# Kernel tuning notes

Hardware: AMD Instinct MI355X
Metric: run time of the kernel (lower is better)

## Reference

```python
import jax, jax.numpy as jnp
import numpy as np

# ---- config (matches init_kwargs) ----
CLIP_FRAMES, CLIP_STRIDE = 1, 2
CODEBOOK_SIZE, CODEBOOK_DIM = 1024, 512
WORD_SIZE = CODEBOOK_SIZE // 4
VOCAB = 3000
LAMBDA_MMD, LAMBDA_SIM = 0.1, 1.0


def conv3d(x, w, b, pad):
    # x: (N,C,T,H,W), w: (O,I,kt,kh,kw)
    out = jax.lax.conv_general_dilated(x, w, (1, 1, 1), [(p, p) for p in pad],
                                       dimension_numbers=('NCDHW', 'OIDHW', 'NCDHW'))
    return out + b[None, :, None, None, None]


def bn_relu(x, g, b, nc):
    # training-mode BatchNorm3d, stats computed per clip-batch (over B,T,H,W),
    # matching the torch loop that calls the encoder once per clip.
    s = x.shape
    xr = x.reshape((nc, s[0] // nc) + s[1:])
    m = xr.mean(axis=(1, 3, 4, 5), keepdims=True)
    v = xr.var(axis=(1, 3, 4, 5), keepdims=True)
    xn = (xr - m) * jax.lax.rsqrt(v + 1e-5)
    xn = xn * g[None, None, :, None, None, None] + b[None, None, :, None, None, None]
    return jax.nn.relu(xn).reshape(s)


def maxpool_hw(x):
    return jax.lax.reduce_window(x, -jnp.inf, jax.lax.max,
                                 (1, 1, 1, 2, 2), (1, 1, 1, 2, 2), 'VALID')


def gru_layer(x, w_ih, w_hh, b_ih, b_hh):
    # PyTorch GRU cell math; x: (B,L,D) -> (B,L,H)
    B = x.shape[0]
    H = w_hh.shape[1]

    def step(h, xt):
        gi = xt @ w_ih.T + b_ih
        gh = h @ w_hh.T + b_hh
        i_r, i_z, i_n = jnp.split(gi, 3, axis=-1)
        h_r, h_z, h_n = jnp.split(gh, 3, axis=-1)
        r = jax.nn.sigmoid(i_r + h_r)
        z = jax.nn.sigmoid(i_z + h_z)
        n = jnp.tanh(i_n + r * h_n)
        hn = (1.0 - z) * n + z * h
        return hn, hn

    h0 = jnp.zeros((B, H), x.dtype)
    _, ys = jax.lax.scan(step, h0, jnp.swapaxes(x, 0, 1))
    return jnp.swapaxes(ys, 0, 1)


def nearest_code(flat, book):
    # squared euclidean distance; argmin identical to torch.cdist(p=2)+argmin
    d2 = (flat * flat).sum(-1, keepdims=True) - 2.0 * flat @ book.T + (book * book).sum(-1)
    return jnp.argmin(d2, axis=-1)


def _forward(videos, conv1_w, conv1_b, bn1_g, bn1_b, conv2_w, conv2_b, bn2_g, bn2_b,
             conv3_w, conv3_b, bn3_g, bn3_b, tconv_w, tconv_b, bn4_g, bn4_b,
             proj_w, proj_b, codebook, word_codebook, align_w, align_b,
             gru_wih0, gru_whh0, gru_bih0, gru_bhh0, gru_wih1, gru_whh1, gru_bih1, gru_bhh1,
             dec1_w, dec1_b, dec2_w, dec2_b, dec3_w, dec3_b, text_tokens):
    sg = jax.lax.stop_gradient
    B, _, T, Hh, Ww = videos.shape
    nc = (T - CLIP_FRAMES) // CLIP_STRIDE + 1
    # gather all clips, fold clip dim into batch for the convs
    idx = jnp.arange(nc)[:, None] * CLIP_STRIDE + jnp.arange(CLIP_FRAMES)[None]
    clips = jnp.transpose(videos[:, :, idx], (2, 0, 1, 3, 4, 5))  # (nc,B,3,cf,H,W)
    x = clips.reshape(nc * B, 3, CLIP_FRAMES, Hh, Ww)
    x = maxpool_hw(bn_relu(conv3d(x, conv1_w, conv1_b, (1, 1, 1)), bn1_g, bn1_b, nc))
    x = maxpool_hw(bn_relu(conv3d(x, conv2_w, conv2_b, (1, 1, 1)), bn2_g, bn2_b, nc))
    x = bn_relu(conv3d(x, conv3_w, conv3_b, (1, 1, 1)), bn3_g, bn3_b, nc)
    # AdaptiveAvgPool3d((CLIP_FRAMES,4,4)): T already CLIP_FRAMES, H,W divisible by 4
    N, C, Tc, Hc, Wc = x.shape
    x = x.reshape(N, C, Tc, 4, Hc // 4, 4, Wc // 4).mean(axis=(4, 6))
    x = bn_relu(conv3d(x, tconv_w, tconv_b, (1, 0, 0)), bn4_g, bn4_b, nc)
    feats = jnp.transpose(x.reshape(nc, B, -1), (1, 0, 2))  # (B, nc, 256*cf*16)
    features = feats @ proj_w.T + proj_b                     # (B, nc, D)
    D = features.shape[-1]
    # --- VQ quantize ---
    flat = features.reshape(-1, D)
    tok = nearest_code(flat, codebook)
    quantized = codebook[tok].reshape(B, nc, D)
    commitment = jnp.mean((features - sg(quantized)) ** 2)
    codebook_loss = jnp.mean((quantized - sg(features)) ** 2)
    h = gru_layer(quantized[:, :-1], gru_wih0, gru_whh0, gru_bih0, gru_bhh0)
    h = gru_layer(h, gru_wih1, gru_whh1, gru_bih1, gru_bhh1)
    context_loss = jnp.mean((h - features[:, 1:]) ** 2)
    vq_loss = commitment + 0.25 * codebook_loss + 0.1 * context_loss
    # --- SimpleCRA: mean of char pairs -> nearest word code ---
    wsrc = quantized.reshape(B, nc // 2, 2, D).mean(axis=2)
    widx = nearest_code(wsrc.reshape(-1, D), word_codebook).reshape(B, nc // 2)
    wemb = word_codebook[widx]  # (B, nw, D)
    flat_w = wemb.reshape(-1, D)
    alignment = jnp.mean((flat_w @ align_w.T + align_b - sg(flat_w)) ** 2)
    # --- translation: mean word context -> MLP decoder -> CE vs first token, summed over batch ---
    ctx = wemb.mean(axis=1)  # (B, D)
    hh = jax.nn.relu(ctx @ dec1_w.T + dec1_b)
    hh = jax.nn.relu(hh @ dec2_w.T + dec2_b)  # dropout = identity (eval)
    logits = hh @ dec3_w.T + dec3_b           # (B, VOCAB)
    logp = jax.nn.log_softmax(logits, axis=-1)
    translation = -jnp.take_along_axis(logp, text_tokens[:, :1], axis=1).sum()
    total = vq_loss + LAMBDA_MMD * alignment + LAMBDA_SIM * translation
    return widx, total


def setup_inputs() -> dict:
    key = jax.random.key(0)
    ks = iter(jax.random.split(key, 48))

    def rn(shape, scale):
        return jax.random.normal(next(ks), shape, jnp.float32) * scale

    D = CODEBOOK_DIM
    inp = {}
    inp['videos'] = jax.random.normal(next(ks), (4, 3, 32, 64, 64), jnp.float32)
    inp['conv1_w'] = rn((64, 3, 3, 3, 3), 0.15); inp['conv1_b'] = jnp.zeros((64,), jnp.float32)
    inp['bn1_g'] = jnp.ones((64,), jnp.float32); inp['bn1_b'] = jnp.zeros((64,), jnp.float32)
    inp['conv2_w'] = rn((128, 64, 3, 3, 3), 0.034); inp['conv2_b'] = jnp.zeros((128,), jnp.float32)
    inp['bn2_g'] = jnp.ones((128,), jnp.float32); inp['bn2_b'] = jnp.zeros((128,), jnp.float32)
    inp['conv3_w'] = rn((256, 128, 3, 3, 3), 0.024); inp['conv3_b'] = jnp.zeros((256,), jnp.float32)
    inp['bn3_g'] = jnp.ones((256,), jnp.float32); inp['bn3_b'] = jnp.zeros((256,), jnp.float32)
    inp['tconv_w'] = rn((256, 256, 3, 1, 1), 0.05); inp['tconv_b'] = jnp.zeros((256,), jnp.float32)
    inp['bn4_g'] = jnp.ones((256,), jnp.float32); inp['bn4_b'] = jnp.zeros((256,), jnp.float32)
    inp['proj_w'] = rn((D, 256 * CLIP_FRAMES * 16), 0.02); inp['proj_b'] = jnp.zeros((D,), jnp.float32)
    inp['codebook'] = jax.random.uniform(next(ks), (CODEBOOK_SIZE, D), jnp.float32,
                                         -1.0 / CODEBOOK_SIZE, 1.0 / CODEBOOK_SIZE)
    inp['word_codebook'] = jax.random.uniform(next(ks), (WORD_SIZE, D), jnp.float32,
                                              -1.0 / WORD_SIZE, 1.0 / WORD_SIZE)
    inp['align_w'] = rn((D, D), 0.04); inp['align_b'] = jnp.zeros((D,), jnp.float32)
    for l in (0, 1):
        inp[f'gru_wih{l}'] = rn((3 * D, D), 0.044)
        inp[f'gru_whh{l}'] = rn((3 * D, D), 0.044)
        inp[f'gru_bih{l}'] = jnp.zeros((3 * D,), jnp.float32)
        inp[f'gru_bhh{l}'] = jnp.zeros((3 * D,), jnp.float32)
    inp['dec1_w'] = rn((512, D), 0.044); inp['dec1_b'] = jnp.zeros((512,), jnp.float32)
    inp['dec2_w'] = rn((1024, 512), 0.044); inp['dec2_b'] = jnp.zeros((1024,), jnp.float32)
    inp['dec3_w'] = rn((VOCAB, 1024), 0.031); inp['dec3_b'] = jnp.zeros((VOCAB,), jnp.float32)
    inp['text_tokens'] = jax.random.randint(next(ks), (4, 10), 0, VOCAB)
    return inp


def reference(videos, conv1_w, conv1_b, bn1_g, bn1_b, conv2_w, conv2_b, bn2_g, bn2_b,
              conv3_w, conv3_b, bn3_g, bn3_b, tconv_w, tconv_b, bn4_g, bn4_b,
              proj_w, proj_b, codebook, word_codebook, align_w, align_b,
              gru_wih0, gru_whh0, gru_bih0, gru_bhh0, gru_wih1, gru_whh1, gru_bih1, gru_bhh1,
              dec1_w, dec1_b, dec2_w, dec2_b, dec3_w, dec3_b, text_tokens):
    return _forward(videos, conv1_w, conv1_b, bn1_g, bn1_b, conv2_w, conv2_b, bn2_g, bn2_b,
                    conv3_w, conv3_b, bn3_g, bn3_b, tconv_w, tconv_b, bn4_g, bn4_b,
                    proj_w, proj_b, codebook, word_codebook, align_w, align_b,
                    gru_wih0, gru_whh0, gru_bih0, gru_bhh0, gru_wih1, gru_whh1, gru_bih1, gru_bhh1,
                    dec1_w, dec1_b, dec2_w, dec2_b, dec3_w, dec3_b, text_tokens)
```

## Files before the change

kernel.cpp:

```cpp
#include <hip/hip_runtime.h>


static const size_t OFF_X1P  = 0;
static const size_t OFF_Y2   = 4194304;
static const size_t OFF_X2P  = 0;
static const size_t OFF_Y3   = 4194304;
static const size_t OFF_Y3P1 = 8388608;
static const size_t OFF_X3P  = 2097152;
static const size_t OFF_Y4   = 2359296;
static const size_t OFF_X4   = 2621440;
static const size_t OFF_FEAT = 2883584;
static const size_t OFF_QUANT= 2916352;
static const size_t OFF_GI1  = 2949120;
static const size_t OFF_GI2  = 3047424;
static const size_t OFF_H1   = 3145728;
static const size_t OFF_H2   = 3178496;
static const size_t OFF_WEMB = 3211264;
static const size_t OFF_CTX  = 3227648;
static const size_t OFF_HH1  = 3229696;
static const size_t OFF_HH2  = 3231744;
static const size_t OFF_LOG  = 3235840;
static const size_t OFF_PP   = 3247840;
static const size_t OFF_SC    = 12582912;
static const size_t OFF_SH    = 12587008;
static const size_t OFF_ACCP  = 12591104;
static const size_t OFF_COMMIT= 12623872;
static const size_t OFF_CTXA  = 12623936;
static const size_t OFF_ALIGNA= 12624056;

__global__ __launch_bounds__(256) void k_conv1_stats3(
        const float* __restrict__ videos, const float* __restrict__ w1,
        const float* __restrict__ b1, float* __restrict__ accP) {
    __shared__ float sP[3 * 18 * 66];
    __shared__ float wsm[3 * 9 * 16];
    __shared__ float sRed[4][16], qRed[4][16];
    int oc0 = blockIdx.x * 16, rq = blockIdx.y, n = blockIdx.z;
    int c = n >> 2, b = n & 3;
    int tid = threadIdx.x;
    int rp = tid >> 5, cq = tid & 31;
    for (int e = tid; e < 3564; e += 256) {
        int ic = e / 1188, rem = e % 1188;
        int r = rem / 66, col = rem % 66;
        int gr = rq * 16 - 1 + r, gc = col - 1;
        float v = 0.f;
        if (gr >= 0 && gr < 64 && gc >= 0 && gc < 64)
            v = videos[((size_t)(b * 3 + ic) * 32 + 2 * c) * 4096 + gr * 64 + gc];
        sP[e] = v;
    }
    for (int e = tid; e < 432; e += 256) {
        int ic = e / 144, rem = e % 144, k = rem / 16, j = rem % 16;
        wsm[e] = w1[((size_t)((oc0 + j) * 3 + ic) * 3 + 1) * 9 + k];
    }
    __syncthreads();
    float acc[4][16];
#pragma unroll
    for (int p = 0; p < 4; ++p)
#pragma unroll
        for (int j = 0; j < 16; ++j) acc[p][j] = 0.f;
#pragma unroll
    for (int ic = 0; ic < 3; ++ic) {
        const float* base = &sP[ic * 1188 + (2 * rp) * 66 + 2 * cq];
        float patch[4][4];
#pragma unroll
        for (int r = 0; r < 4; ++r)
#pragma unroll
            for (int q = 0; q < 4; ++q) patch[r][q] = base[r * 66 + q];
#pragma unroll
        for (int k = 0; k < 9; ++k) {
            int kr = k / 3, kc = k % 3;
            float4 w0 = *(const float4*)&wsm[(ic * 9 + k) * 16 + 0];
            float4 w1v = *(const float4*)&wsm[(ic * 9 + k) * 16 + 4];
            float4 w2 = *(const float4*)&wsm[(ic * 9 + k) * 16 + 8];
            float4 w3 = *(const float4*)&wsm[(ic * 9 + k) * 16 + 12];
#pragma unroll
            for (int p = 0; p < 4; ++p) {
                float vv = patch[(p >> 1) + kr][(p & 1) + kc];
                acc[p][0]  += vv * w0.x; acc[p][1]  += vv * w0.y;
                acc[p][2]  += vv * w0.z; acc[p][3]  += vv * w0.w;
                acc[p][4]  += vv * w1v.x; acc[p][5]  += vv * w1v.y;
                acc[p][6]  += vv * w1v.z; acc[p][7]  += vv * w1v.w;
                acc[p][8]  += vv * w2.x; acc[p][9]  += vv * w2.y;
                acc[p][10] += vv * w2.z; acc[p][11] += vv * w2.w;
                acc[p][12] += vv * w3.x; acc[p][13] += vv * w3.y;
                acc[p][14] += vv * w3.z; acc[p][15] += vv * w3.w;
            }
        }
    }
    int lane = tid & 63, wave = tid >> 6;
#pragma unroll
    for (int j = 0; j < 16; ++j) {
        float bj = b1[oc0 + j];
        float s = 0.f, q = 0.f;
#pragma unroll
        for (int p = 0; p < 4; ++p) {
            float a = acc[p][j] + bj;
            s += a; q += a * a;
        }
#pragma unroll
        for (int m = 1; m < 64; m <<= 1) {
            s += __shfl_xor(s, m);
            q += __shfl_xor(q, m);
        }
        if (lane == 0) { sRed[wave][j] = s; qRed[wave][j] = q; }
    }
    __syncthreads();
    if (tid < 16) {
        float s = ((sRed[0][tid] + sRed[1][tid]) + (sRed[2][tid] + sRed[3][tid]));
        float q = ((qRed[0][tid] + qRed[1][tid]) + (qRed[2][tid] + qRed[3][tid]));
        int oc = oc0 + tid;
        size_t slot = (((size_t)(c * 64 + oc)) * 4 + b) * 4 + rq;
        accP[slot] = s;
        accP[16384 + slot] = q;
    }
}

__global__ void k_conv1_fin(const float* __restrict__ accP, const float* __restrict__ g1,
                            const float* __restrict__ be1, float* __restrict__ sc,
                            float* __restrict__ sh) {
    int e = blockIdx.x * 256 + threadIdx.x;
    if (e >= 1024) return;
    int oc = e & 63;
    const float* ps = accP + (size_t)e * 16;
    const float* pq = accP + 16384 + (size_t)e * 16;
    float s = 0.f, q = 0.f;
#pragma unroll
    for (int i = 0; i < 16; ++i) { s += ps[i]; q += pq[i]; }
    float m = s * (1.f / 16384.f);
    float var = q * (1.f / 16384.f) - m * m;
    float sf = g1[oc] * rsqrtf(var + 1e-5f);
    sc[e] = sf;
    sh[e] = be1[oc] - m * sf;
}

__global__ __launch_bounds__(256) void k_conv1_apply3(
        const float* __restrict__ videos, const float* __restrict__ w1,
        const float* __restrict__ b1, const float* __restrict__ sc,
        const float* __restrict__ sh, float* __restrict__ x1p) {
    __shared__ float sP[3 * 18 * 66];
    __shared__ float wsm[3 * 9 * 16];
    int oc0 = blockIdx.x * 16, rq = blockIdx.y, n = blockIdx.z;
    int c = n >> 2, b = n & 3;
    int tid = threadIdx.x;
    int rp = tid >> 5, cq = tid & 31;
    for (int e = tid; e < 3564; e += 256) {
        int ic = e / 1188, rem = e % 1188;
        int r = rem / 66, col = rem % 66;
        int gr = rq * 16 - 1 + r, gc = col - 1;
        float v = 0.f;
        if (gr >= 0 && gr < 64 && gc >= 0 && gc < 64)
            v = videos[((size_t)(b * 3 + ic) * 32 + 2 * c) * 4096 + gr * 64 + gc];
        sP[e] = v;
    }
    for (int e = tid; e < 432; e += 256) {
        int ic = e / 144, rem = e % 144, k = rem / 16, j = rem % 16;
        wsm[e] = w1[((size_t)((oc0 + j) * 3 + ic) * 3 + 1) * 9 + k];
    }
    __syncthreads();
    float acc[4][16];
#pragma unroll
    for (int p = 0; p < 4; ++p)
#pragma unroll
        for (int j = 0; j < 16; ++j) acc[p][j] = 0.f;
#pragma unroll
    for (int ic = 0; ic < 3; ++ic) {
        const float* base = &sP[ic * 1188 + (2 * rp) * 66 + 2 * cq];
        float patch[4][4];
#pragma unroll
        for (int r = 0; r < 4; ++r)
#pragma unroll
            for (int q = 0; q < 4; ++q) patch[r][q] = base[r * 66 + q];
#pragma unroll
        for (int k = 0; k < 9; ++k) {
            int kr = k / 3, kc = k % 3;
            float4 w0 = *(const float4*)&wsm[(ic * 9 + k) * 16 + 0];
            float4 w1v = *(const float4*)&wsm[(ic * 9 + k) * 16 + 4];
            float4 w2 = *(const float4*)&wsm[(ic * 9 + k) * 16 + 8];
            float4 w3 = *(const float4*)&wsm[(ic * 9 + k) * 16 + 12];
#pragma unroll
            for (int p = 0; p < 4; ++p) {
                float vv = patch[(p >> 1) + kr][(p & 1) + kc];
                acc[p][0]  += vv * w0.x; acc[p][1]  += vv * w0.y;
                acc[p][2]  += vv * w0.z; acc[p][3]  += vv * w0.w;
                acc[p][4]  += vv * w1v.x; acc[p][5]  += vv * w1v.y;
                acc[p][6]  += vv * w1v.z; acc[p][7]  += vv * w1v.w;
                acc[p][8]  += vv * w2.x; acc[p][9]  += vv * w2.y;
                acc[p][10] += vv * w2.z; acc[p][11] += vv * w2.w;
                acc[p][12] += vv * w3.x; acc[p][13] += vv * w3.y;
                acc[p][14] += vv * w3.z; acc[p][15] += vv * w3.w;
            }
        }
    }
#pragma unroll
    for (int j = 0; j < 16; ++j) {
        int oc = oc0 + j;
        float bj = b1[oc];
        float scj = sc[c * 64 + oc], shj = sh[c * 64 + oc];
        float m = -1e30f;
#pragma unroll
        for (int p = 0; p < 4; ++p) m = fmaxf(m, (acc[p][j] + bj) * scj + shj);
        x1p[((size_t)n * 64 + oc) * 1024 + (rq * 8 + rp) * 32 + cq] = fmaxf(m, 0.f);
    }
}

__global__ __launch_bounds__(256) void k_conv2(
        const float* __restrict__ in, const float* __restrict__ wt,
        const float* __restrict__ bias, float* __restrict__ out) {
    __shared__ __align__(16) float sIn[8 * 10 * 36];
    __shared__ __align__(16) float sW[8 * 9 * 32];
    int oc0 = blockIdx.x * 32, r0 = blockIdx.y * 8, n = blockIdx.z;
    int tid = threadIdx.x;
    int ocq = tid >> 5;
    int rg = (tid >> 3) & 3;
    int cg = tid & 7;
    float acc[4][8];
#pragma unroll
    for (int j = 0; j < 4; ++j)
#pragma unroll
        for (int p = 0; p < 8; ++p) acc[j][p] = 0.f;

    for (int ic0 = 0; ic0 < 64; ic0 += 8) {
        __syncthreads();
        for (int e = tid; e < 2720; e += 256) {
            int ch = e / 340, rem = e % 340;
            int r = rem / 34, col = rem % 34;
            int gr = r0 - 1 + r, gc = col - 1;
            float v = 0.f;
            if (gr >= 0 && gr < 32 && gc >= 0 && gc < 32)
                v = in[((size_t)(n * 64 + ic0 + ch) * 32 + gr) * 32 + gc];
            sIn[ch * 360 + r * 36 + col] = v;
        }
        for (int e = tid; e < 2304; e += 256) {
            int c = e / 288, r1 = e % 288, k = r1 / 32, j = r1 % 32;
            sW[e] = wt[((size_t)(oc0 + j) * 64 + ic0 + c) * 27 + 9 + k];
        }
        __syncthreads();
        for (int c = 0; c < 8; ++c) {
            const float* base = &sIn[c * 360 + (2 * rg) * 36 + 4 * cg];
            float patch[4][6];
#pragma unroll
            for (int r = 0; r < 4; ++r) {
                float4 p4 = *(const float4*)&base[r * 36];
                float2 p2 = *(const float2*)&base[r * 36 + 4];
                patch[r][0] = p4.x; patch[r][1] = p4.y; patch[r][2] = p4.z;
                patch[r][3] = p4.w; patch[r][4] = p2.x; patch[r][5] = p2.y;
            }
#pragma unroll
            for (int k = 0; k < 9; ++k) {
                int kr = k / 3, kc = k % 3;
                float4 w4 = *(const float4*)&sW[c * 288 + k * 32 + ocq * 4];
#pragma unroll
                for (int p = 0; p < 8; ++p) {
                    int pr = p >> 2, pcq = p & 3;
                    float vv = patch[pr + kr][pcq + kc];
                    acc[0][p] += vv * w4.x; acc[1][p] += vv * w4.y;
                    acc[2][p] += vv * w4.z; acc[3][p] += vv * w4.w;
                }
            }
        }
    }
#pragma unroll
    for (int j = 0; j < 4; ++j) {
        int oc = oc0 + ocq * 4 + j;
        float bj = bias[oc];
#pragma unroll
        for (int pr = 0; pr < 2; ++pr) {
            float4 o4 = make_float4(acc[j][pr * 4 + 0] + bj, acc[j][pr * 4 + 1] + bj,
                                    acc[j][pr * 4 + 2] + bj, acc[j][pr * 4 + 3] + bj);
            *(float4*)&out[((size_t)(n * 128 + oc) * 32 + r0 + 2 * rg + pr) * 32 + 4 * cg] = o4;
        }
    }
}

__global__ __launch_bounds__(256) void k_conv3p(
        const float* __restrict__ in, const float* __restrict__ wt,
        float* __restrict__ outP) {
    __shared__ __align__(16) float sIn[8 * 18 * 20];
    __shared__ __align__(16) float sW[8 * 9 * 32];
    int oc0 = blockIdx.x * 32, n = blockIdx.y, half = blockIdx.z;
    int tid = threadIdx.x;
    int ocq = tid >> 5;
    int rg = (tid >> 2) & 7;
    int cg = tid & 3;
    float acc[4][8];
#pragma unroll
    for (int j = 0; j < 4; ++j)
#pragma unroll
        for (int p = 0; p < 8; ++p) acc[j][p] = 0.f;

    int icB = half * 64;
    for (int ic0 = icB; ic0 < icB + 64; ic0 += 8) {
        __syncthreads();
        for (int e = tid; e < 2592; e += 256) {
            int ch = e / 324, rem = e % 324;
            int r = rem / 18, cc = rem % 18;
            int gr = r - 1, gc = cc - 1;
            float v = 0.f;
            if (gr >= 0 && gr < 16 && gc >= 0 && gc < 16)
                v = in[((size_t)(n * 128 + ic0 + ch) * 16 + gr) * 16 + gc];
            sIn[ch * 360 + r * 20 + cc] = v;
        }
        for (int e = tid; e < 2304; e += 256) {
            int c = e / 288, r1 = e % 288, k = r1 / 32, j = r1 % 32;
            sW[e] = wt[((size_t)(oc0 + j) * 128 + ic0 + c) * 27 + 9 + k];
        }
        __syncthreads();
        for (int c = 0; c < 8; ++c) {
            const float* base = &sIn[c * 360 + (2 * rg) * 20 + 4 * cg];
            float patch[4][6];
#pragma unroll
            for (int r = 0; r < 4; ++r) {
                float4 p4 = *(const float4*)&base[r * 20];
                float2 p2 = *(const float2*)&base[r * 20 + 4];
                patch[r][0] = p4.x; patch[r][1] = p4.y; patch[r][2] = p4.z;
                patch[r][3] = p4.w; patch[r][4] = p2.x; patch[r][5] = p2.y;
            }
#pragma unroll
            for (int k = 0; k < 9; ++k) {
                int kr = k / 3, kc = k % 3;
                float4 w4 = *(const float4*)&sW[c * 288 + k * 32 + ocq * 4];
#pragma unroll
                for (int p = 0; p < 8; ++p) {
                    int pr = p >> 2, pcq = p & 3;
                    float vv = patch[pr + kr][pcq + kc];
                    acc[0][p] += vv * w4.x; acc[1][p] += vv * w4.y;
                    acc[2][p] += vv * w4.z; acc[3][p] += vv * w4.w;
                }
            }
        }
    }
    float* dst = outP + (size_t)half * 4194304;
#pragma unroll
    for (int j = 0; j < 4; ++j) {
        int oc = oc0 + ocq * 4 + j;
#pragma unroll
        for (int pr = 0; pr < 2; ++pr) {
            float4 o4 = make_float4(acc[j][pr * 4 + 0], acc[j][pr * 4 + 1],
                                    acc[j][pr * 4 + 2], acc[j][pr * 4 + 3]);
            *(float4*)&dst[((size_t)(n * 256 + oc) * 16 + 2 * rg + pr) * 16 + 4 * cg] = o4;
        }
    }
}

__global__ void k_bn_stats3p(const float* __restrict__ P, const float* __restrict__ bias,
                             const float* __restrict__ g, const float* __restrict__ be,
                             float* __restrict__ scale, float* __restrict__ shift) {
    int c = blockIdx.x, ch = blockIdx.y, tid = threadIdx.x;
    float bj = bias[ch];
    float s = 0.f, s2 = 0.f;
    for (int b = 0; b < 4; ++b) {
        size_t base = ((size_t)(c * 4 + b) * 256 + ch) * 256;
        for (int i = tid; i < 256; i += 256) {
            size_t idx = base + i;
            float v = (P[idx] + P[idx + 4194304]) + bj;
            s += v; s2 += v * v;
        }
    }
    __shared__ float rs[256], rq[256];
    rs[tid] = s; rq[tid] = s2; __syncthreads();
    for (int k = 128; k > 0; k >>= 1) {
        if (tid < k) { rs[tid] += rs[tid + k]; rq[tid] += rq[tid + k]; }
        __syncthreads();
    }
    if (tid == 0) {
        float inv = 1.f / 1024.f;
        float m = rs[0] * inv, var = rq[0] * inv - m * m;
        float sc = g[ch] * rsqrtf(var + 1e-5f);
        scale[c * 256 + ch] = sc;
        shift[c * 256 + ch] = be[ch] - m * sc;
    }
}

__global__ void k_bn_apply_avgpool4p(const float* __restrict__ P, const float* __restrict__ bias,
                                     const float* __restrict__ scale, const float* __restrict__ shift,
                                     float* __restrict__ out) {
    size_t idx = (size_t)blockIdx.x * 256 + threadIdx.x;
    int j = (int)(idx & 3), i = (int)(idx >> 2) & 3;
    int ch = (int)(idx >> 4) & 255, n = (int)(idx >> 12);
    int c = n >> 2;
    float bj = bias[ch];
    float sc = scale[c * 256 + ch], sh = shift[c * 256 + ch];
    size_t base = (((size_t)n * 256 + ch) * 16 + i * 4) * 16 + j * 4;
    float s = 0.f;
#pragma unroll
    for (int r = 0; r < 4; ++r)
#pragma unroll
        for (int q = 0; q < 4; ++q) {
            size_t pidx = base + r * 16 + q;
            float v = (P[pidx] + P[pidx + 4194304]) + bj;
            s += fmaxf(v * sc + sh, 0.f);
        }
    out[idx] = s * (1.f / 16.f);
}

__global__ void k_bn_stats(const float* __restrict__ buf, const float* __restrict__ g,
                           const float* __restrict__ be, float* __restrict__ scale,
                           float* __restrict__ shift, int C, int HW) {
    int c = blockIdx.x, ch = blockIdx.y, tid = threadIdx.x;
    float s = 0.f, s2 = 0.f;
    for (int b = 0; b < 4; ++b) {
        const float* p = buf + ((size_t)(c * 4 + b) * C + ch) * HW;
        for (int i = tid; i < HW; i += 256) { float v = p[i]; s += v; s2 += v * v; }
    }
    __shared__ float rs[256], rq[256];
    rs[tid] = s; rq[tid] = s2; __syncthreads();
    for (int k = 128; k > 0; k >>= 1) {
        if (tid < k) { rs[tid] += rs[tid + k]; rq[tid] += rq[tid + k]; }
        __syncthreads();
    }
    if (tid == 0) {
        float inv = 1.f / (float)(4 * HW);
        float m = rs[0] * inv, var = rq[0] * inv - m * m;
        float sc = g[ch] * rsqrtf(var + 1e-5f);
        scale[c * C + ch] = sc;
        shift[c * C + ch] = be[ch] - m * sc;
    }
}

__global__ void k_bn_apply_pool(const float* __restrict__ in, const float* __restrict__ scale,
                                const float* __restrict__ shift, float* __restrict__ out,
                                int C, int H, int W) {
    int OH = H >> 1, OW = W >> 1;
    size_t idx = (size_t)blockIdx.x * 256 + threadIdx.x;
    int ow = (int)(idx % OW);
    size_t r = idx / OW;
    int oh = (int)(r % OH); r /= OH;
    int ch = (int)(r % C);
    int n = (int)(r / C);
    int c = n >> 2;
    float sc = scale[c * C + ch], sh = shift[c * C + ch];
    const float* p = in + (((size_t)n * C + ch) * H + 2 * oh) * W + 2 * ow;
    float m = 0.f;
    m = fmaxf(m, p[0] * sc + sh);
    m = fmaxf(m, p[1] * sc + sh);
    m = fmaxf(m, p[W] * sc + sh);
    m = fmaxf(m, p[W + 1] * sc + sh);
    out[idx] = m;
}

__global__ void k_tconv(const float* __restrict__ x3p, const float* __restrict__ tw,
                        const float* __restrict__ tb, float* __restrict__ y4) {
    size_t idx = (size_t)blockIdx.x * 256 + threadIdx.x;
    int p = (int)(idx & 15), o = (int)(idx >> 4) & 255, n = (int)(idx >> 12);
    const float* xr = x3p + (size_t)n * 4096 + p;
    float a = tb[o];
    for (int i = 0; i < 256; ++i) a += xr[i * 16] * tw[((size_t)o * 256 + i) * 3 + 1];
    y4[idx] = a;
}

__global__ void k_bn_apply(const float* __restrict__ in, const float* __restrict__ scale,
                           const float* __restrict__ shift, float* __restrict__ out) {
    size_t idx = (size_t)blockIdx.x * 256 + threadIdx.x;
    int ch = (int)(idx >> 4) & 255, n = (int)(idx >> 12);
    int c = n >> 2;
    float sc = scale[c * 256 + ch], sh = shift[c * 256 + ch];
    out[idx] = fmaxf(in[idx] * sc + sh, 0.f);
}

__global__ __launch_bounds__(256) void k_proj_part(
        const float* __restrict__ A, const float* __restrict__ B, float* __restrict__ PP) {
    __shared__ __align__(16) float As[64 * 68];
    __shared__ __align__(16) float Bs[64 * 68];
    int n0 = blockIdx.x * 64, ks = blockIdx.y;
    int tid = threadIdx.x, tm = tid >> 4, tn = tid & 15;
    float acc[4][4];
#pragma unroll
    for (int i = 0; i < 4; ++i)
#pragma unroll
        for (int j = 0; j < 4; ++j) acc[i][j] = 0.f;
    int kb = ks * 512;
    for (int k0 = kb; k0 < kb + 512; k0 += 64) {
        __syncthreads();
        for (int e = tid; e < 4096; e += 256) {
            int m = e >> 6, k = e & 63;
            As[k * 68 + m] = A[(size_t)m * 4096 + k0 + k];
            Bs[k * 68 + m] = B[(size_t)(n0 + m) * 4096 + k0 + k];
        }
        __syncthreads();
        for (int k = 0; k < 64; ++k) {
            float4 a4 = *(const float4*)&As[k * 68 + tm * 4];
            float4 b4 = *(const float4*)&Bs[k * 68 + tn * 4];
            acc[0][0] += a4.x * b4.x; acc[0][1] += a4.x * b4.y;
            acc[0][2] += a4.x * b4.z; acc[0][3] += a4.x * b4.w;
            acc[1][0] += a4.y * b4.x; acc[1][1] += a4.y * b4.y;
            acc[1][2] += a4.y * b4.z; acc[1][3] += a4.y * b4.w;
            acc[2][0] += a4.z * b4.x; acc[2][1] += a4.z * b4.y;
            acc[2][2] += a4.z * b4.z; acc[2][3] += a4.z * b4.w;
            acc[3][0] += a4.w * b4.x; acc[3][1] += a4.w * b4.y;
            acc[3][2] += a4.w * b4.z; acc[3][3] += a4.w * b4.w;
        }
    }
#pragma unroll
    for (int i = 0; i < 4; ++i)
#pragma unroll
        for (int j = 0; j < 4; ++j)
            PP[((size_t)(ks * 64 + tm * 4 + i)) * 512 + n0 + tn * 4 + j] = acc[i][j];
}

__global__ void k_proj_fin(const float* __restrict__ PP, const float* __restrict__ pb,
                           float* __restrict__ feat) {
    int e = blockIdx.x * 256 + threadIdx.x;
    int n = e & 511;
    int m = e >> 9;
    float s = pb[n];
#pragma unroll
    for (int ks = 0; ks < 8; ++ks) s += PP[(size_t)ks * 32768 + e];
    int c = m >> 2, b = m & 3;
    int ro = b * 16 + c;
    feat[(size_t)ro * 512 + n] = s;
}

__global__ void k_vq(const float* __restrict__ feat, const float* __restrict__ cb,
                     float* __restrict__ quant, float* __restrict__ commitArr) {
    int row = blockIdx.x, tid = threadIdx.x;
    __shared__ float f[512];
    for (int k = tid; k < 512; k += 256) f[k] = feat[(size_t)row * 512 + k];
    __syncthreads();
    float best = 3.4e38f; int bidx = 0;
    for (int j = tid; j < 1024; j += 256) {
        const float* c = cb + (size_t)j * 512;
        float d2 = 0.f;
        for (int k = 0; k < 512; ++k) { float t = f[k] - c[k]; d2 += t * t; }
        if (d2 < best) { best = d2; bidx = j; }
    }
    __shared__ float rd[256]; __shared__ int ri[256];
    rd[tid] = best; ri[tid] = bidx; __syncthreads();
    for (int k = 128; k > 0; k >>= 1) {
        if (tid < k) {
            float od = rd[tid + k]; int oi = ri[tid + k];
            if (od < rd[tid] || (od == rd[tid] && oi < ri[tid])) { rd[tid] = od; ri[tid] = oi; }
        }
        __syncthreads();
    }
    __shared__ int wsel;
    if (tid == 0) { wsel = ri[0]; commitArr[row] = rd[0]; }
    __syncthreads();
    const float* c = cb + (size_t)wsel * 512;
    for (int k = tid; k < 512; k += 256) quant[(size_t)row * 512 + k] = c[k];
}

__device__ __forceinline__ void gru_gi_one(
        const float* __restrict__ xsRow, const float* __restrict__ wih,
        const float* __restrict__ bih, float* __restrict__ gi, int row, int d) {
    const float4* xp = (const float4*)xsRow;
    const float4* wr = (const float4*)(wih + (size_t)d * 512);
    float a0 = 0.f, a1 = 0.f, a2 = 0.f, a3 = 0.f;
    for (int i = 0; i < 128; i += 4) {
        float4 w0 = wr[i], w1 = wr[i + 1], w2 = wr[i + 2], w3 = wr[i + 3];
        float4 x0 = xp[i], x1 = xp[i + 1], x2 = xp[i + 2], x3 = xp[i + 3];
        a0 += w0.x * x0.x + w0.y * x0.y + w0.z * x0.z + w0.w * x0.w;
        a1 += w1.x * x1.x + w1.y * x1.y + w1.z * x1.z + w1.w * x1.w;
        a2 += w2.x * x2.x + w2.y * x2.y + w2.z * x2.z + w2.w * x2.w;
        a3 += w3.x * x3.x + w3.y * x3.y + w3.z * x3.z + w3.w * x3.w;
    }
    gi[(size_t)row * 1536 + d] = (a0 + a1) + (a2 + a3) + bih[d];
}

__device__ __forceinline__ void gru_step_body(
        const float* __restrict__ gi, const float* __restrict__ whh,
        const float* __restrict__ bhh, float* __restrict__ hseq, int t, int blk) {
    int wv = threadIdx.x >> 6, lane = threadIdx.x & 63;
    int d = blk * 4 + wv;
    const float4* w0p = (const float4*)(whh + (size_t)d * 512);
    const float4* w1p = (const float4*)(whh + (size_t)(512 + d) * 512);
    const float4* w2p = (const float4*)(whh + (size_t)(1024 + d) * 512);
    float4 w0a = w0p[lane * 2], w0b = w0p[lane * 2 + 1];
    float4 w1a = w1p[lane * 2], w1b = w1p[lane * 2 + 1];
    float4 w2a = w2p[lane * 2], w2b = w2p[lane * 2 + 1];
    float bh0 = bhh[d], bh1 = bhh[512 + d], bh2 = bhh[1024 + d];
    for (int b = 0; b < 4; ++b) {
        float4 ha = make_float4(0, 0, 0, 0), hb = ha;
        float hpd = 0.f;
        if (t > 0) {
            const float4* hp = (const float4*)(hseq + (size_t)(b * 16 + t - 1) * 512);
            ha = hp[lane * 2]; hb = hp[lane * 2 + 1];
            hpd = hseq[(size_t)(b * 16 + t - 1) * 512 + d];
        }
        float s0 = w0a.x * ha.x + w0a.y * ha.y + w0a.z * ha.z + w0a.w * ha.w
                 + w0b.x * hb.x + w0b.y * hb.y + w0b.z * hb.z + w0b.w * hb.w;
        float s1 = w1a.x * ha.x + w1a.y * ha.y + w1a.z * ha.z + w1a.w * ha.w
                 + w1b.x * hb.x + w1b.y * hb.y + w1b.z * hb.z + w1b.w * hb.w;
        float s2 = w2a.x * ha.x + w2a.y * ha.y + w2a.z * ha.z + w2a.w * ha.w
                 + w2b.x * hb.x + w2b.y * hb.y + w2b.z * hb.z + w2b.w * hb.w;
#pragma unroll
        for (int m = 1; m < 64; m <<= 1) {
            s0 += __shfl_xor(s0, m);
            s1 += __shfl_xor(s1, m);
            s2 += __shfl_xor(s2, m);
        }
        const float* gr = gi + (size_t)(b * 16 + t) * 1536;
        float rr = 1.f / (1.f + expf(-(gr[d] + s0 + bh0)));
        float zz = 1.f / (1.f + expf(-(gr[512 + d] + s1 + bh1)));
        float nn = tanhf(gr[1024 + d] + rr * (s2 + bh2));
        if (lane == 0)
            hseq[(size_t)(b * 16 + t) * 512 + d] = (1.f - zz) * nn + zz * hpd;
    }
}

__global__ void k_gru_gi6(const float* __restrict__ x, const float* __restrict__ wih,
                          const float* __restrict__ bih, float* __restrict__ gi) {
    int g = blockIdx.x;
    int r = g / 6, part = g % 6;
    int b = r / 15, t = r % 15;
    int row = b * 16 + t;
    __shared__ float xsRow[512];
    for (int k = threadIdx.x; k < 512; k += 256) xsRow[k] = x[(size_t)row * 512 + k];
    __syncthreads();
    gru_gi_one(xsRow, wih, bih, gi, row, part * 256 + threadIdx.x);
}

__global__ __launch_bounds__(256) void k_gru_pipe(
        const float* __restrict__ gi1, const float* __restrict__ whh0,
        const float* __restrict__ bhh0, float* __restrict__ h1,
        const float* __restrict__ wih1, const float* __restrict__ bih1,
        float* __restrict__ gi2, const float* __restrict__ whh1,
        const float* __restrict__ bhh1, float* __restrict__ h2, int t) {
    int bid = blockIdx.x;
    if (bid < 128) {
        if (t < 15) gru_step_body(gi1, whh0, bhh0, h1, t, bid);
    } else if (bid < 256) {
        if (t >= 2) gru_step_body(gi2, whh1, bhh1, h2, t - 2, bid - 128);
    } else {
        if (t >= 1 && t <= 15) {
            int local = bid - 256;
            int b = local / 6, part = local % 6;
            int row = b * 16 + (t - 1);
            __shared__ float xsRow[512];
            for (int k = threadIdx.x; k < 512; k += 256)
                xsRow[k] = h1[(size_t)row * 512 + k];
            __syncthreads();
            gru_gi_one(xsRow, wih1, bih1, gi2, row, part * 256 + threadIdx.x);
        }
    }
}

__global__ void k_ctx_loss(const float* __restrict__ h2, const float* __restrict__ feat,
                           float* __restrict__ ctxArr) {
    int tid = threadIdx.x;
    size_t idx = (size_t)blockIdx.x * 256 + tid;
    int d = (int)(idx & 511);
    int rt = (int)(idx >> 9);
    int t = rt % 15, b = rt / 15;
    float diff = h2[(size_t)(b * 16 + t) * 512 + d] - feat[(size_t)(b * 16 + t + 1) * 512 + d];
    float v = diff * diff;
#pragma unroll
    for (int m = 1; m < 64; m <<= 1) v += __shfl_xor(v, m);
    __shared__ float ws[4];
    if ((tid & 63) == 0) ws[tid >> 6] = v;
    __syncthreads();
    if (tid == 0) ctxArr[blockIdx.x] = ((ws[0] + ws[1]) + (ws[2] + ws[3]));
}

__global__ void k_word_vq(const float* __restrict__ quant, const float* __restrict__ wcb,
                          float* __restrict__ wemb, float* __restrict__ out_widx) {
    int row = blockIdx.x;
    int b = row >> 3, wi = row & 7;
    int tid = threadIdx.x;
    __shared__ float f[512];
    for (int k = tid; k < 512; k += 256)
        f[k] = 0.5f * (quant[(size_t)(b * 16 + 2 * wi) * 512 + k] +
                       quant[(size_t)(b * 16 + 2 * wi + 1) * 512 + k]);
    __syncthreads();
    const float* cp = wcb + (size_t)tid * 512;
    float d2 = 0.f;
    for (int k = 0; k < 512; ++k) { float t = f[k] - cp[k]; d2 += t * t; }
    __shared__ float rd[256]; __shared__ int ri[256];
    rd[tid] = d2; ri[tid] = tid; __syncthreads();
    for (int k = 128; k > 0; k >>= 1) {
        if (tid < k) {
            float od = rd[tid + k]; int oi = ri[tid + k];
            if (od < rd[tid] || (od == rd[tid] && oi < ri[tid])) { rd[tid] = od; ri[tid] = oi; }
        }
        __syncthreads();
    }
    __shared__ int wsel;
    if (tid == 0) { wsel = ri[0]; out_widx[row] = (float)ri[0]; }
    __syncthreads();
    const float* cb = wcb + (size_t)wsel * 512;
    for (int k = tid; k < 512; k += 256) wemb[(size_t)row * 512 + k] = cb[k];
}

__global__ void k_align(const float* __restrict__ wemb, const float* __restrict__ aw,
                        const float* __restrict__ ab, float* __restrict__ alignArr) {
    int row = blockIdx.x, tid = threadIdx.x;
    __shared__ float e[512];
    for (int k = tid; k < 512; k += 256) e[k] = wemb[(size_t)row * 512 + k];
    __syncthreads();
    float local = 0.f;
    for (int d = tid; d < 512; d += 256) {
        const float* wr = aw + (size_t)d * 512;
        float a = ab[d] - e[d];
        for (int k = 0; k < 512; ++k) a += e[k] * wr[k];
        local += a * a;
    }
    __shared__ float rs[256];
    rs[tid] = local; __syncthreads();
    for (int k = 128; k > 0; k >>= 1) { if (tid < k) rs[tid] += rs[tid + k]; __syncthreads(); }
    if (tid == 0) alignArr[row] = rs[0];
}

__global__ void k_ctx(const float* __restrict__ wemb, float* __restrict__ ctx) {
    int e = blockIdx.x * 256 + threadIdx.x;
    int b = e >> 9, d = e & 511;
    float s = 0.f;
#pragma unroll
    for (int wi = 0; wi < 8; ++wi) s += wemb[(size_t)(b * 8 + wi) * 512 + d];
    ctx[e] = s * 0.125f;
}

__global__ void k_smallM(const float* __restrict__ A, const float* __restrict__ B,
                         const float* __restrict__ bias, float* __restrict__ C,
                         int N, int K, int relu) {
    __shared__ float xs[4096];
    int tid = threadIdx.x;
    for (int e = tid; e < 4 * K; e += 256) xs[e] = A[e];
    __syncthreads();
    int r = tid >> 4, kt = tid & 15;
    int n = blockIdx.x * 16 + r;
    float acc[4] = {0, 0, 0, 0};
    if (n < N) {
        int iters = K >> 6;
        for (int i = 0; i < iters; ++i) {
            int k = i * 64 + kt * 4;
            float4 w = *(const float4*)&B[(size_t)n * K + k];
#pragma unroll
            for (int b = 0; b < 4; ++b) {
                float4 x = *(const float4*)&xs[b * K + k];
                acc[b] += w.x * x.x + w.y * x.y + w.z * x.z + w.w * x.w;
            }
        }
    }
#pragma unroll
    for (int b = 0; b < 4; ++b) {
#pragma unroll
        for (int m = 1; m < 16; m <<= 1) acc[b] += __shfl_xor(acc[b], m);
    }
    if (kt == 0 && n < N) {
#pragma unroll
        for (int b = 0; b < 4; ++b) {
            float v = acc[b] + bias[n];
            if (relu) v = fmaxf(v, 0.f);
            C[(size_t)b * N + n] = v;
        }
    }
}

__global__ void k_final(const float* __restrict__ logits, const int* __restrict__ tokens,
                        const float* __restrict__ commitArr, const float* __restrict__ ctxArr,
                        const float* __restrict__ alignArr, float* __restrict__ out_total) {
    int tid = threadIdx.x;
    __shared__ float rs[256];
    __shared__ float sM;
    float tr = 0.f;
    for (int b = 0; b < 4; ++b) {
        const float* lg = logits + (size_t)b * 3000;
        float m = -1e30f;
        for (int d = tid; d < 3000; d += 256) m = fmaxf(m, lg[d]);
        rs[tid] = m; __syncthreads();
        for (int k = 128; k > 0; k >>= 1) { if (tid < k) rs[tid] = fmaxf(rs[tid], rs[tid + k]); __syncthreads(); }
        if (tid == 0) sM = rs[0];
        __syncthreads();
        float M = sM;
        float s = 0.f;
        for (int d = tid; d < 3000; d += 256) s += expf(lg[d] - M);
        rs[tid] = s; __syncthreads();
        for (int k = 128; k > 0; k >>= 1) { if (tid < k) rs[tid] += rs[tid + k]; __syncthreads(); }
        if (tid == 0) {
            int t0 = tokens[b * 10];
            tr += -(lg[t0] - M - logf(rs[0]));
        }
        __syncthreads();
    }
    if (tid == 0) {
        float c0 = 0.f;
        for (int i = 0; i < 64; ++i) c0 += commitArr[i];
        float c1 = 0.f;
        for (int i = 0; i < 120; ++i) c1 += ctxArr[i];
        float c2 = 0.f;
        for (int i = 0; i < 32; ++i) c2 += alignArr[i];
        float total = 1.25f * c0 * (1.f / 32768.f)
                    + 0.1f  * c1 * (1.f / 30720.f)
                    + 0.1f  * c2 * (1.f / 16384.f)
                    + tr;
        *out_total = total;
    }
}

extern "C" void kernel_launch(void* const* d_in, const int* in_sizes, int n_in,
                              void* d_out, int out_size, void* d_ws, size_t ws_size,
                              hipStream_t stream) {
    (void)in_sizes; (void)n_in; (void)out_size; (void)ws_size;
    const float* videos   = (const float*)d_in[0];
    const float* conv1_w  = (const float*)d_in[1];
    const float* conv1_b  = (const float*)d_in[2];
    const float* bn1_g    = (const float*)d_in[3];
    const float* bn1_b    = (const float*)d_in[4];
    const float* conv2_w  = (const float*)d_in[5];
    const float* conv2_b  = (const float*)d_in[6];
    const float* bn2_g    = (const float*)d_in[7];
    const float* bn2_b    = (const float*)d_in[8];
    const float* conv3_w  = (const float*)d_in[9];
    const float* conv3_b  = (const float*)d_in[10];
    const float* bn3_g    = (const float*)d_in[11];
    const float* bn3_b    = (const float*)d_in[12];
    const float* tconv_w  = (const float*)d_in[13];
    const float* tconv_b  = (const float*)d_in[14];
    const float* bn4_g    = (const float*)d_in[15];
    const float* bn4_b    = (const float*)d_in[16];
    const float* proj_w   = (const float*)d_in[17];
    const float* proj_b   = (const float*)d_in[18];
    const float* codebook = (const float*)d_in[19];
    const float* word_cb  = (const float*)d_in[20];
    const float* align_w  = (const float*)d_in[21];
    const float* align_b  = (const float*)d_in[22];
    const float* gru_wih0 = (const float*)d_in[23];
    const float* gru_whh0 = (const float*)d_in[24];
    const float* gru_bih0 = (const float*)d_in[25];
    const float* gru_bhh0 = (const float*)d_in[26];
    const float* gru_wih1 = (const float*)d_in[27];
    const float* gru_whh1 = (const float*)d_in[28];
    const float* gru_bih1 = (const float*)d_in[29];
    const float* gru_bhh1 = (const float*)d_in[30];
    const float* dec1_w   = (const float*)d_in[31];
    const float* dec1_b   = (const float*)d_in[32];
    const float* dec2_w   = (const float*)d_in[33];
    const float* dec2_b   = (const float*)d_in[34];
    const float* dec3_w   = (const float*)d_in[35];
    const float* dec3_b   = (const float*)d_in[36];
    const int*   tokens   = (const int*)d_in[37];

    float* wsf    = (float*)d_ws;
    float* out    = (float*)d_out;
    float* x1p    = wsf + OFF_X1P;
    float* x2p    = wsf + OFF_X2P;
    float* y2     = wsf + OFF_Y2;
    float* y3     = wsf + OFF_Y3;
    float* x3p    = wsf + OFF_X3P;
    float* y4     = wsf + OFF_Y4;
    float* x4     = wsf + OFF_X4;
    float* feat   = wsf + OFF_FEAT;
    float* quant  = wsf + OFF_QUANT;
    float* gi1    = wsf + OFF_GI1;
    float* gi2    = wsf + OFF_GI2;
    float* h1     = wsf + OFF_H1;
    float* h2     = wsf + OFF_H2;
    float* wemb   = wsf + OFF_WEMB;
    float* ctx    = wsf + OFF_CTX;
    float* hh1    = wsf + OFF_HH1;
    float* hh2    = wsf + OFF_HH2;
    float* logit  = wsf + OFF_LOG;
    float* pp     = wsf + OFF_PP;
    float* sc     = wsf + OFF_SC;
    float* sh     = wsf + OFF_SH;
    float* accP   = wsf + OFF_ACCP;
    float* commitA= wsf + OFF_COMMIT;
    float* ctxA   = wsf + OFF_CTXA;
    float* alignA = wsf + OFF_ALIGNA;

    k_conv1_stats3<<<dim3(4, 4, 64), 256, 0, stream>>>(videos, conv1_w, conv1_b, accP);
    k_conv1_fin<<<4, 256, 0, stream>>>(accP, bn1_g, bn1_b, sc, sh);
    k_conv1_apply3<<<dim3(4, 4, 64), 256, 0, stream>>>(videos, conv1_w, conv1_b, sc, sh, x1p);
    k_conv2<<<dim3(4, 4, 64), 256, 0, stream>>>(x1p, conv2_w, conv2_b, y2);
    k_bn_stats<<<dim3(16, 128), 256, 0, stream>>>(y2, bn2_g, bn2_b, sc, sh, 128, 1024);
    k_bn_apply_pool<<<8192, 256, 0, stream>>>(y2, sc, sh, x2p, 128, 32, 32);
    k_conv3p<<<dim3(8, 64, 2), 256, 0, stream>>>(x2p, conv3_w, y3);
    k_bn_stats3p<<<dim3(16, 256), 256, 0, stream>>>(y3, conv3_b, bn3_g, bn3_b, sc, sh);
    k_bn_apply_avgpool4p<<<1024, 256, 0, stream>>>(y3, conv3_b, sc, sh, x3p);
    k_tconv<<<1024, 256, 0, stream>>>(x3p, tconv_w, tconv_b, y4);
    k_bn_stats<<<dim3(16, 256), 256, 0, stream>>>(y4, bn4_g, bn4_b, sc, sh, 256, 16);
    k_bn_apply<<<1024, 256, 0, stream>>>(y4, sc, sh, x4);
    k_proj_part<<<dim3(8, 8), 256, 0, stream>>>(x4, proj_w, pp);
    k_proj_fin<<<128, 256, 0, stream>>>(pp, proj_b, feat);
    k_vq<<<64, 256, 0, stream>>>(feat, codebook, quant, commitA);
    k_gru_gi6<<<360, 256, 0, stream>>>(quant, gru_wih0, gru_bih0, gi1);
    for (int t = 0; t <= 16; ++t)
        k_gru_pipe<<<280, 256, 0, stream>>>(gi1, gru_whh0, gru_bhh0, h1,
                                            gru_wih1, gru_bih1, gi2,
                                            gru_whh1, gru_bhh1, h2, t);
    k_ctx_loss<<<120, 256, 0, stream>>>(h2, feat, ctxA);
    k_word_vq<<<32, 256, 0, stream>>>(quant, word_cb, wemb, out);
    k_align<<<32, 256, 0, stream>>>(wemb, align_w, align_b, alignA);
    k_ctx<<<8, 256, 0, stream>>>(wemb, ctx);
    k_smallM<<<32, 256, 0, stream>>>(ctx, dec1_w, dec1_b, hh1, 512, 512, 1);
    k_smallM<<<64, 256, 0, stream>>>(hh1, dec2_w, dec2_b, hh2, 1024, 512, 1);
    k_smallM<<<188, 256, 0, stream>>>(hh2, dec3_w, dec3_b, logit, 3000, 1024, 0);
    k_final<<<1, 256, 0, stream>>>(logit, tokens, commitA, ctxA, alignA, out + 32);
}
```

Before: 1.095 ms.

## Fold word-VQ and decoder chain into GRU timestep pipeline kernel

Moves word VQ, alignment loss, context averaging and the three decoder matmuls into extra blocks of the per-timestep GRU pipeline kernel, one stage per timestep. The independent decoder chain then overlaps with the latency-bound GRU recurrence, and six separate kernel launches go away. The cost is a larger grid and more shared memory per block in every GRU step launch, which could slow the critical GRU blocks.

```diff
diff --git a/kernel.cpp b/kernel.cpp
--- a/kernel.cpp
+++ b/kernel.cpp
@@ -596,6 +596,44 @@
     }
 }
 
+__device__ __forceinline__ void dev_smallM(float* xs, const float* __restrict__ A,
+                                           const float* __restrict__ B,
+                                           const float* __restrict__ bias,
+                                           float* __restrict__ C,
+                                           int N, int K, int relu, int blk) {
+    int tid = threadIdx.x;
+    for (int e = tid; e < 4 * K; e += 256) xs[e] = A[e];
+    __syncthreads();
+    int r = tid >> 4, kt = tid & 15;
+    int n = blk * 16 + r;
+    float acc[4] = {0, 0, 0, 0};
+    if (n < N) {
+        int iters = K >> 6;
+        for (int i = 0; i < iters; ++i) {
+            int k = i * 64 + kt * 4;
+            float4 w = *(const float4*)&B[(size_t)n * K + k];
+#pragma unroll
+            for (int b = 0; b < 4; ++b) {
+                float4 x = *(const float4*)&xs[b * K + k];
+                acc[b] += w.x * x.x + w.y * x.y + w.z * x.z + w.w * x.w;
+            }
+        }
+    }
+#pragma unroll
+    for (int b = 0; b < 4; ++b) {
+#pragma unroll
+        for (int m = 1; m < 16; m <<= 1) acc[b] += __shfl_xor(acc[b], m);
+    }
+    if (kt == 0 && n < N) {
+#pragma unroll
+        for (int b = 0; b < 4; ++b) {
+            float v = acc[b] + bias[n];
+            if (relu) v = fmaxf(v, 0.f);
+            C[(size_t)b * N + n] = v;
+        }
+    }
+}
+
 __global__ void k_gru_gi6(const float* __restrict__ x, const float* __restrict__ wih,
                           const float* __restrict__ bih, float* __restrict__ gi) {
     int g = blockIdx.x;
@@ -613,22 +651,98 @@
         const float* __restrict__ bhh0, float* __restrict__ h1,
         const float* __restrict__ wih1, const float* __restrict__ bih1,
         float* __restrict__ gi2, const float* __restrict__ whh1,
-        const float* __restrict__ bhh1, float* __restrict__ h2, int t) {
+        const float* __restrict__ bhh1, float* __restrict__ h2,
+        const float* __restrict__ quant, const float* __restrict__ wcb,
+        float* __restrict__ wemb, float* __restrict__ out_widx,
+        const float* __restrict__ aw, const float* __restrict__ ab,
+        float* __restrict__ alignArr, float* __restrict__ ctxB,
+        const float* __restrict__ dec1_w, const float* __restrict__ dec1_b,
+        float* __restrict__ hh1, const float* __restrict__ dec2_w,
+        const float* __restrict__ dec2_b, float* __restrict__ hh2,
+        const float* __restrict__ dec3_w, const float* __restrict__ dec3_b,
+        float* __restrict__ logit, int t) {
+    __shared__ float shbuf[4096];
+    __shared__ float redf[256];
+    __shared__ int   redi[256];
+    __shared__ int   wsel_s;
     int bid = blockIdx.x;
+    int tid = threadIdx.x;
     if (bid < 128) {
         if (t < 15) gru_step_body(gi1, whh0, bhh0, h1, t, bid);
     } else if (bid < 256) {
         if (t >= 2) gru_step_body(gi2, whh1, bhh1, h2, t - 2, bid - 128);
-    } else {
+    } else if (bid < 280) {
         if (t >= 1 && t <= 15) {
             int local = bid - 256;
             int b = local / 6, part = local % 6;
             int row = b * 16 + (t - 1);
-            __shared__ float xsRow[512];
-            for (int k = threadIdx.x; k < 512; k += 256)
-                xsRow[k] = h1[(size_t)row * 512 + k];
+            for (int k = tid; k < 512; k += 256)
+                shbuf[k] = h1[(size_t)row * 512 + k];
             __syncthreads();
-            gru_gi_one(xsRow, wih1, bih1, gi2, row, part * 256 + threadIdx.x);
+            gru_gi_one(shbuf, wih1, bih1, gi2, row, part * 256 + tid);
+        }
+    } else {
+        int tb = bid - 280;
+        if (t == 0) {
+            if (tb < 32) {
+                int b = tb >> 3, wi = tb & 7;
+                for (int k = tid; k < 512; k += 256)
+                    shbuf[k] = 0.5f * (quant[(size_t)(b * 16 + 2 * wi) * 512 + k] +
+                                       quant[(size_t)(b * 16 + 2 * wi + 1) * 512 + k]);
+                __syncthreads();
+                const float* cp = wcb + (size_t)tid * 512;
+                float d2 = 0.f;
+                for (int k = 0; k < 512; ++k) { float tt = shbuf[k] - cp[k]; d2 += tt * tt; }
+                redf[tid] = d2; redi[tid] = tid; __syncthreads();
+                for (int k = 128; k > 0; k >>= 1) {
+                    if (tid < k) {
+                        float od = redf[tid + k]; int oi = redi[tid + k];
+                        if (od < redf[tid] || (od == redf[tid] && oi < redi[tid])) {
+                            redf[tid] = od; redi[tid] = oi;
+                        }
+                    }
+                    __syncthreads();
+                }
+                if (tid == 0) { wsel_s = redi[0]; out_widx[tb] = (float)redi[0]; }
+                __syncthreads();
+                const float* cb = wcb + (size_t)wsel_s * 512;
+                for (int k = tid; k < 512; k += 256)
+                    wemb[(size_t)tb * 512 + k] = cb[k];
+            }
+        } else if (t == 1) {
+            if (tb < 32) {
+                for (int k = tid; k < 512; k += 256)
+                    shbuf[k] = wemb[(size_t)tb * 512 + k];
+                __syncthreads();
+                float local = 0.f;
+                for (int d = tid; d < 512; d += 256) {
+                    const float* wr = aw + (size_t)d * 512;
+                    float a = ab[d] - shbuf[d];
+                    for (int k = 0; k < 512; ++k) a += shbuf[k] * wr[k];
+                    local += a * a;
+                }
+                redf[tid] = local; __syncthreads();
+                for (int k = 128; k > 0; k >>= 1) {
+                    if (tid < k) redf[tid] += redf[tid + k];
+                    __syncthreads();
+                }
+                if (tid == 0) alignArr[tb] = redf[0];
+            }
+        } else if (t == 2) {
+            if (tb < 8) {
+                int e = tb * 256 + tid;
+                int b = e >> 9, d = e & 511;
+                float s = 0.f;
+#pragma unroll
+                for (int wi = 0; wi < 8; ++wi) s += wemb[(size_t)(b * 8 + wi) * 512 + d];
+                ctxB[e] = s * 0.125f;
+            }
+        } else if (t == 3) {
+            if (tb < 32) dev_smallM(shbuf, ctxB, dec1_w, dec1_b, hh1, 512, 512, 1, tb);
+        } else if (t == 4) {
+            if (tb < 64) dev_smallM(shbuf, hh1, dec2_w, dec2_b, hh2, 1024, 512, 1, tb);
+        } else if (t == 5) {
+            if (tb < 188) dev_smallM(shbuf, hh2, dec3_w, dec3_b, logit, 3000, 1024, 0, tb);
         }
     }
 }
@@ -648,100 +762,6 @@
     if ((tid & 63) == 0) ws[tid >> 6] = v;
     __syncthreads();
     if (tid == 0) ctxArr[blockIdx.x] = ((ws[0] + ws[1]) + (ws[2] + ws[3]));
-}
-
-__global__ void k_word_vq(const float* __restrict__ quant, const float* __restrict__ wcb,
-                          float* __restrict__ wemb, float* __restrict__ out_widx) {
-    int row = blockIdx.x;
-    int b = row >> 3, wi = row & 7;
-    int tid = threadIdx.x;
-    __shared__ float f[512];
-    for (int k = tid; k < 512; k += 256)
-        f[k] = 0.5f * (quant[(size_t)(b * 16 + 2 * wi) * 512 + k] +
-                       quant[(size_t)(b * 16 + 2 * wi + 1) * 512 + k]);
-    __syncthreads();
-    const float* cp = wcb + (size_t)tid * 512;
-    float d2 = 0.f;
-    for (int k = 0; k < 512; ++k) { float t = f[k] - cp[k]; d2 += t * t; }
-    __shared__ float rd[256]; __shared__ int ri[256];
-    rd[tid] = d2; ri[tid] = tid; __syncthreads();
-    for (int k = 128; k > 0; k >>= 1) {
-        if (tid < k) {
-            float od = rd[tid + k]; int oi = ri[tid + k];
-            if (od < rd[tid] || (od == rd[tid] && oi < ri[tid])) { rd[tid] = od; ri[tid] = oi; }
-        }
-        __syncthreads();
-    }
-    __shared__ int wsel;
-    if (tid == 0) { wsel = ri[0]; out_widx[row] = (float)ri[0]; }
-    __syncthreads();
-    const float* cb = wcb + (size_t)wsel * 512;
-    for (int k = tid; k < 512; k += 256) wemb[(size_t)row * 512 + k] = cb[k];
-}
-
-__global__ void k_align(const float* __restrict__ wemb, const float* __restrict__ aw,
-                        const float* __restrict__ ab, float* __restrict__ alignArr) {
-    int row = blockIdx.x, tid = threadIdx.x;
-    __shared__ float e[512];
-    for (int k = tid; k < 512; k += 256) e[k] = wemb[(size_t)row * 512 + k];
-    __syncthreads();
-    float local = 0.f;
-    for (int d = tid; d < 512; d += 256) {
-        const float* wr = aw + (size_t)d * 512;
-        float a = ab[d] - e[d];
-        for (int k = 0; k < 512; ++k) a += e[k] * wr[k];
-        local += a * a;
-    }
-    __shared__ float rs[256];
-    rs[tid] = local; __syncthreads();
-    for (int k = 128; k > 0; k >>= 1) { if (tid < k) rs[tid] += rs[tid + k]; __syncthreads(); }
-    if (tid == 0) alignArr[row] = rs[0];
-}
-
-__global__ void k_ctx(const float* __restrict__ wemb, float* __restrict__ ctx) {
-    int e = blockIdx.x * 256 + threadIdx.x;
-    int b = e >> 9, d = e & 511;
-    float s = 0.f;
-#pragma unroll
-    for (int wi = 0; wi < 8; ++wi) s += wemb[(size_t)(b * 8 + wi) * 512 + d];
-    ctx[e] = s * 0.125f;
-}
-
-__global__ void k_smallM(const float* __restrict__ A, const float* __restrict__ B,
-                         const float* __restrict__ bias, float* __restrict__ C,
-                         int N, int K, int relu) {
-    __shared__ float xs[4096];
-    int tid = threadIdx.x;
-    for (int e = tid; e < 4 * K; e += 256) xs[e] = A[e];
-    __syncthreads();
-    int r = tid >> 4, kt = tid & 15;
-    int n = blockIdx.x * 16 + r;
-    float acc[4] = {0, 0, 0, 0};
-    if (n < N) {
-        int iters = K >> 6;
-        for (int i = 0; i < iters; ++i) {
-            int k = i * 64 + kt * 4;
-            float4 w = *(const float4*)&B[(size_t)n * K + k];
-#pragma unroll
-            for (int b = 0; b < 4; ++b) {
-                float4 x = *(const float4*)&xs[b * K + k];
-                acc[b] += w.x * x.x + w.y * x.y + w.z * x.z + w.w * x.w;
-            }
-        }
-    }
-#pragma unroll
-    for (int b = 0; b < 4; ++b) {
-#pragma unroll
-        for (int m = 1; m < 16; m <<= 1) acc[b] += __shfl_xor(acc[b], m);
-    }
-    if (kt == 0 && n < N) {
-#pragma unroll
-        for (int b = 0; b < 4; ++b) {
-            float v = acc[b] + bias[n];
-            if (relu) v = fmaxf(v, 0.f);
-            C[(size_t)b * N + n] = v;
-        }
-    }
 }
 
 __global__ void k_final(const float* __restrict__ logits, const int* __restrict__ tokens,
@@ -873,15 +893,14 @@
     k_vq<<<64, 256, 0, stream>>>(feat, codebook, quant, commitA);
     k_gru_gi6<<<360, 256, 0, stream>>>(quant, gru_wih0, gru_bih0, gi1);
     for (int t = 0; t <= 16; ++t)
-        k_gru_pipe<<<280, 256, 0, stream>>>(gi1, gru_whh0, gru_bhh0, h1,
+        k_gru_pipe<<<468, 256, 0, stream>>>(gi1, gru_whh0, gru_bhh0, h1,
                                             gru_wih1, gru_bih1, gi2,
-                                            gru_whh1, gru_bhh1, h2, t);
+                                            gru_whh1, gru_bhh1, h2,
+                                            quant, word_cb, wemb, out,
+                                            align_w, align_b, alignA, ctx,
+                                            dec1_w, dec1_b, hh1,
+                                            dec2_w, dec2_b, hh2,
+                                            dec3_w, dec3_b, logit, t);
     k_ctx_loss<<<120, 256, 0, stream>>>(h2, feat, ctxA);
-    k_word_vq<<<32, 256, 0, stream>>>(quant, word_cb, wemb, out);
-    k_align<<<32, 256, 0, stream>>>(wemb, align_w, align_b, alignA);
-    k_ctx<<<8, 256, 0, stream>>>(wemb, ctx);
-    k_smallM<<<32, 256, 0, stream>>>(ctx, dec1_w, dec1_b, hh1, 512, 512, 1);
-    k_smallM<<<64, 256, 0, stream>>>(hh1, dec2_w, dec2_b, hh2, 1024, 512, 1);
-    k_smallM<<<188, 256, 0, stream>>>(hh2, dec3_w, dec3_b, logit, 3000, 1024, 0);
     k_final<<<1, 256, 0, stream>>>(logit, tokens, commitA, ctxA, alignA, out + 32);
 }
```

After: 1.046 ms, median of 2. 1.05x faster.
